# Optimization experiments

Measured on AMD Instinct MI355X. Metric: run time of the kernel, lower is better.

The kernel has to match this reference:

```python
import jax, jax.numpy as jnp
import numpy as np

N_NODES = 100000
N_EDGES = 1600000
IN_DIM = 128
OUT_DIM = 64


def setup_inputs() -> dict:
    key = jax.random.key(0)
    k1, k2, k3, k4 = jax.random.split(key, 4)
    h = jax.random.normal(k1, (N_NODES, IN_DIM), dtype=jnp.float32)
    W = jax.random.normal(k2, (OUT_DIM, IN_DIM), dtype=jnp.float32) * (1.0 / np.sqrt(IN_DIM))
    a_w = jax.random.normal(k3, (1, 2 * OUT_DIM), dtype=jnp.float32) * (1.0 / np.sqrt(2 * OUT_DIM))
    edge_index = jax.random.randint(k4, (2, N_EDGES), 0, N_NODES, dtype=jnp.int64 if jax.config.jax_enable_x64 else jnp.int32)
    return {"h": h, "W": W, "a_w": a_w, "edge_index": edge_index}


def reference(h, W, a_w, edge_index):
    # Wh: [N, out_dim]  (Linear without bias: x @ W.T)
    Wh = h @ W.T
    src, dst = edge_index[0], edge_index[1]
    # per-edge concat [Wh[src], Wh[dst]] -> [E, 2*out_dim]
    e = jnp.concatenate([Wh[src], Wh[dst]], axis=-1)
    # attention logits: [E]
    alpha = jax.nn.leaky_relu(e @ a_w.T, negative_slope=0.2)[:, 0]
    # global-max-stabilized exp (matches the torch code exactly)
    alpha_exp = jnp.exp(alpha - jnp.max(alpha))
    # segment softmax denominator over destination nodes: [N]
    alpha_sum = jax.ops.segment_sum(alpha_exp, dst, num_segments=N_NODES)
    alpha_norm = alpha_exp / (alpha_sum[dst] + 1e-9)
    # weighted scatter-add aggregation: [N, out_dim]
    out = jax.ops.segment_sum(alpha_norm[:, None] * Wh[src], dst, num_segments=N_NODES)
    return (jax.nn.elu(out), alpha_norm)
```

## Files before the change

kernel.cpp:

```cpp
#include <hip/hip_runtime.h>
#include <math.h>

#define N_NODES 100000
#define N_EDGES 1600000
#define IN_DIM 128
#define OUT_DIM 64

#define BSHIFT 9
#define BSIZE  (1 << BSHIFT)
#define NB     ((N_NODES + BSIZE - 1) >> BSHIFT)
#define EDGES_PER_BLK 2048
#define NBLK   ((N_EDGES + EDGES_PER_BLK - 1) / EDGES_PER_BLK)
#define SCANA_LEN (NB * NBLK)
#define SCANA_ITEMS 1024
#define SCANA_NB ((SCANA_LEN + SCANA_ITEMS - 1) / SCANA_ITEMS)

typedef short short8 __attribute__((ext_vector_type(8)));
typedef float f32x4 __attribute__((ext_vector_type(4)));

__device__ __forceinline__ unsigned short f2bf(float x) {
    unsigned int u = __float_as_uint(x);
    return (unsigned short)((u + 0x7FFFu + ((u >> 16) & 1u)) >> 16);
}
__device__ __forceinline__ short8 pack_bf16x8(float4 p, float4 q) {
    short8 r;
    r[0] = (short)f2bf(p.x); r[1] = (short)f2bf(p.y);
    r[2] = (short)f2bf(p.z); r[3] = (short)f2bf(p.w);
    r[4] = (short)f2bf(q.x); r[5] = (short)f2bf(q.y);
    r[6] = (short)f2bf(q.z); r[7] = (short)f2bf(q.w);
    return r;
}

__global__ __launch_bounds__(256) void k_histA(const int* __restrict__ dst,
                                               int* __restrict__ hist_t,
                                               const float* __restrict__ W,
                                               const float* __restrict__ a_w,
                                               float* __restrict__ w1,
                                               float* __restrict__ w2) {
    __shared__ int lhist[NB];
    const int tid = threadIdx.x;
    const int blk = blockIdx.x;
    if (blk == 0 && tid < IN_DIM) {
        float r1 = 0.f, r2 = 0.f;
        #pragma unroll 8
        for (int dd = 0; dd < OUT_DIM; ++dd) {
            float wv = W[dd * IN_DIM + tid];
            r1 = fmaf(a_w[dd], wv, r1);
            r2 = fmaf(a_w[OUT_DIM + dd], wv, r2);
        }
        w1[tid] = r1; w2[tid] = r2;
    }
    if (tid < NB) lhist[tid] = 0;
    __syncthreads();
    const int e0 = blk * EDGES_PER_BLK;
    #pragma unroll
    for (int j = 0; j < 8; ++j) {
        int e = e0 + j * 256 + tid;
        if (e < N_EDGES) atomicAdd(&lhist[dst[e] >> BSHIFT], 1);
    }
    __syncthreads();
    if (tid < NB) hist_t[tid * NBLK + blk] = lhist[tid];
}

__global__ __launch_bounds__(256) void k_wh(const float* __restrict__ h,
                                            const float* __restrict__ W,
                                            const float* __restrict__ w1,
                                            const float* __restrict__ w2,
                                            unsigned short* __restrict__ Wh16,
                                            float* __restrict__ s1,
                                            float* __restrict__ s2) {
    const int tid = threadIdx.x;
    const int wv = tid >> 6;
    const int l  = tid & 63;
    const int g  = l >> 4;
    const int lm = l & 15;
    const int node0 = blockIdx.x * 64 + wv * 16;
    const int row = node0 + lm;
    const int rowc = (row < N_NODES) ? row : (N_NODES - 1);
    const float* hrow = h + (size_t)rowc * IN_DIM;

    short8 afrag[4];
    float sp1 = 0.f, sp2 = 0.f;
    #pragma unroll
    for (int kt = 0; kt < 4; ++kt) {
        const int k0 = kt * 32 + g * 8;
        float4 p = *(const float4*)(hrow + k0);
        float4 q = *(const float4*)(hrow + k0 + 4);
        float4 u1 = *(const float4*)(w1 + k0);
        float4 v1 = *(const float4*)(w1 + k0 + 4);
        float4 u2 = *(const float4*)(w2 + k0);
        float4 v2 = *(const float4*)(w2 + k0 + 4);
        sp1 += p.x*u1.x + p.y*u1.y + p.z*u1.z + p.w*u1.w
             + q.x*v1.x + q.y*v1.y + q.z*v1.z + q.w*v1.w;
        sp2 += p.x*u2.x + p.y*u2.y + p.z*u2.z + p.w*u2.w
             + q.x*v2.x + q.y*v2.y + q.z*v2.z + q.w*v2.w;
        afrag[kt] = pack_bf16x8(p, q);
    }
    sp1 += __shfl_xor(sp1, 16, 64); sp1 += __shfl_xor(sp1, 32, 64);
    sp2 += __shfl_xor(sp2, 16, 64); sp2 += __shfl_xor(sp2, 32, 64);
    if (l < 16 && row < N_NODES) { s1[row] = sp1; s2[row] = sp2; }

    f32x4 acc[4] = {f32x4{0,0,0,0}, f32x4{0,0,0,0}, f32x4{0,0,0,0}, f32x4{0,0,0,0}};
    #pragma unroll
    for (int nt = 0; nt < 4; ++nt) {
        #pragma unroll
        for (int kt = 0; kt < 4; ++kt) {
            const float* wr = W + (size_t)(nt * 16 + lm) * IN_DIM + kt * 32 + g * 8;
            float4 p = *(const float4*)wr;
            float4 q = *(const float4*)(wr + 4);
            short8 bfrag = pack_bf16x8(p, q);
            acc[nt] = __builtin_amdgcn_mfma_f32_16x16x32_bf16(afrag[kt], bfrag, acc[nt], 0, 0, 0);
        }
    }
    #pragma unroll
    for (int nt = 0; nt < 4; ++nt) {
        #pragma unroll
        for (int r = 0; r < 4; ++r) {
            int nodo = node0 + g * 4 + r;
            if (nodo < N_NODES)
                Wh16[(size_t)nodo * OUT_DIM + nt * 16 + lm] = f2bf(acc[nt][r]);
        }
    }
}

__global__ __launch_bounds__(256) void k_scanA_part(const int* __restrict__ in,
                                                    int* __restrict__ bsum) {
    __shared__ int wsum[4];
    const int tid = threadIdx.x;
    const int base = blockIdx.x * SCANA_ITEMS + tid * 4;
    int s = 0;
    #pragma unroll
    for (int j = 0; j < 4; ++j) {
        int i = base + j;
        if (i < SCANA_LEN) s += in[i];
    }
    #pragma unroll
    for (int off = 32; off > 0; off >>= 1) s += __shfl_xor(s, off, 64);
    if ((tid & 63) == 0) wsum[tid >> 6] = s;
    __syncthreads();
    if (tid == 0) bsum[blockIdx.x] = wsum[0] + wsum[1] + wsum[2] + wsum[3];
}

__global__ __launch_bounds__(256) void k_scanA_mid(int* __restrict__ bsum) {
    __shared__ int s[256];
    const int tid = threadIdx.x;
    s[tid] = (tid < SCANA_NB) ? bsum[tid] : 0;
    __syncthreads();
    #pragma unroll
    for (int off = 1; off < 256; off <<= 1) {
        int u = (tid >= off) ? s[tid - off] : 0;
        __syncthreads();
        s[tid] += u;
        __syncthreads();
    }
    if (tid < SCANA_NB) bsum[tid] = (tid > 0) ? s[tid - 1] : 0;
}

__global__ __launch_bounds__(256) void k_scanA_final(const int* __restrict__ in,
                                                     const int* __restrict__ bsum,
                                                     int* __restrict__ outscan) {
    __shared__ int wtot[4];
    const int tid = threadIdx.x;
    const int lane = tid & 63;
    const int wid = tid >> 6;
    const int base = blockIdx.x * SCANA_ITEMS + tid * 4;
    int c[4];
    #pragma unroll
    for (int j = 0; j < 4; ++j)
        c[j] = (base + j < SCANA_LEN) ? in[base + j] : 0;
    int tot = c[0] + c[1] + c[2] + c[3];
    int inc = tot;
    #pragma unroll
    for (int off = 1; off < 64; off <<= 1) {
        int u = __shfl_up(inc, off, 64);
        if (lane >= off) inc += u;
    }
    if (lane == 63) wtot[wid] = inc;
    __syncthreads();
    int wbase = 0;
    #pragma unroll
    for (int w = 0; w < 4; ++w) wbase += (w < wid) ? wtot[w] : 0;
    int run = bsum[blockIdx.x] + wbase + (inc - tot);
    #pragma unroll
    for (int j = 0; j < 4; ++j) {
        int i = base + j;
        if (i < SCANA_LEN) { outscan[i] = run; run += c[j]; }
    }
}

__global__ __launch_bounds__(256) void k_binA(const int* __restrict__ ei,
                                              const float* __restrict__ s1,
                                              const float* __restrict__ s2,
                                              const int* __restrict__ flat_scan,
                                              int2* __restrict__ brec,
                                              float* __restrict__ ae_orig) {
    __shared__ int lbase[NB];
    __shared__ int lcur[NB];
    const int tid = threadIdx.x;
    const int blk = blockIdx.x;
    if (tid < NB) { lbase[tid] = flat_scan[tid * NBLK + blk]; lcur[tid] = 0; }
    __syncthreads();
    const int e0 = blk * EDGES_PER_BLK;
    #pragma unroll
    for (int j = 0; j < 8; ++j) {
        int e = e0 + j * 256 + tid;
        if (e >= N_EDGES) continue;
        int src = ei[e];
        int dst = ei[N_EDGES + e];
        float a = s1[src] + s2[dst];
        a = (a > 0.f) ? a : 0.2f * a;
        float ae = expf(a);
        ae_orig[e] = ae;
        int b = dst >> BSHIFT;
        int r = atomicAdd(&lcur[b], 1);
        brec[lbase[b] + r] = make_int2(src | ((dst & (BSIZE - 1)) << 17),
                                       __float_as_int(ae));
    }
}

__global__ __launch_bounds__(256) void k_fine(const int2* __restrict__ brec,
                                              const int* __restrict__ flat_scan,
                                              int* __restrict__ offsets,
                                              int2* __restrict__ sa_sorted) {
    __shared__ int lhist[BSIZE];
    __shared__ int lofs[BSIZE];
    __shared__ int lcur[BSIZE];
    __shared__ int wsum[4];
    const int tid = threadIdx.x;
    const int lane = tid & 63;
    const int wid = tid >> 6;
    const int b = blockIdx.x;
    const int base = flat_scan[b * NBLK];
    const int endp = (b + 1 < NB) ? flat_scan[(b + 1) * NBLK] : N_EDGES;
    const int cnt = endp - base;
    lhist[tid] = 0; lhist[tid + 256] = 0;
    __syncthreads();
    for (int i = tid; i < cnt; i += 256)
        atomicAdd(&lhist[(unsigned)brec[base + i].x >> 17], 1);
    __syncthreads();
    int c0 = lhist[2 * tid], c1 = lhist[2 * tid + 1];
    int s = c0 + c1;
    int inc = s;
    #pragma unroll
    for (int off = 1; off < 64; off <<= 1) {
        int u = __shfl_up(inc, off, 64);
        if (lane >= off) inc += u;
    }
    if (lane == 63) wsum[wid] = inc;
    __syncthreads();
    int wb = 0;
    #pragma unroll
    for (int w = 0; w < 4; ++w) wb += (w < wid) ? wsum[w] : 0;
    int ex = wb + inc - s;
    lofs[2 * tid] = ex; lofs[2 * tid + 1] = ex + c0;
    lcur[2 * tid] = ex; lcur[2 * tid + 1] = ex + c0;
    __syncthreads();
    const int dst0 = b << BSHIFT;
    #pragma unroll
    for (int j = 0; j < 2; ++j) {
        int jj = tid + j * 256;
        int node = dst0 + jj;
        if (node < N_NODES) offsets[node] = base + lofs[jj];
    }
    if (b == NB - 1 && tid == 0) offsets[N_NODES] = N_EDGES;
    for (int i = tid; i < cnt; i += 256) {
        int2 rec = brec[base + i];
        int dstl = (unsigned)rec.x >> 17;
        int pos = base + atomicAdd(&lcur[dstl], 1);
        sa_sorted[pos] = make_int2(rec.x & 0x1FFFF, rec.y);
    }
}

__global__ __launch_bounds__(256) void k_agg(const int2* __restrict__ sa_sorted,
                                             const int* __restrict__ offsets,
                                             const unsigned short* __restrict__ Wh16,
                                             float* __restrict__ out,
                                             float* __restrict__ inv_tab) {
    const int gid = blockIdx.x * 256 + threadIdx.x;
    const int node = gid >> 6;
    const int l = gid & 63;
    if (node >= N_NODES) return;
    const int g = l >> 3;
    const int o = l & 7;
    const int beg = offsets[node];
    const int end = offsets[node + 1];
    float acc[8] = {0.f, 0.f, 0.f, 0.f, 0.f, 0.f, 0.f, 0.f};
    float S = 0.f;
    int i = beg;
    for (; i + 16 <= end; i += 16) {
        int2 pA = sa_sorted[i + g];
        int2 pB = sa_sorted[i + 8 + g];
        const int4 rA = *(const int4*)(Wh16 + ((size_t)pA.x << 6) + (o << 3));
        const int4 rB = *(const int4*)(Wh16 + ((size_t)pB.x << 6) + (o << 3));
        float aeA = __int_as_float(pA.y);
        float aeB = __int_as_float(pB.y);
        S += aeA + aeB;
        #pragma unroll
        for (int j = 0; j < 4; ++j) {
            int vA = ((const int*)&rA)[j];
            acc[2*j]   = fmaf(aeA, __uint_as_float((unsigned)vA << 16), acc[2*j]);
            acc[2*j+1] = fmaf(aeA, __uint_as_float((unsigned)vA & 0xFFFF0000u), acc[2*j+1]);
        }
        #pragma unroll
        for (int j = 0; j < 4; ++j) {
            int vB = ((const int*)&rB)[j];
            acc[2*j]   = fmaf(aeB, __uint_as_float((unsigned)vB << 16), acc[2*j]);
            acc[2*j+1] = fmaf(aeB, __uint_as_float((unsigned)vB & 0xFFFF0000u), acc[2*j+1]);
        }
    }
    for (; i < end; i += 8) {
        int idx = i + g;
        int2 p = (idx < end) ? sa_sorted[idx] : make_int2(0, 0);
        const int4 r = *(const int4*)(Wh16 + ((size_t)p.x << 6) + (o << 3));
        float ae = __int_as_float(p.y);
        S += ae;
        #pragma unroll
        for (int j = 0; j < 4; ++j) {
            int v = ((const int*)&r)[j];
            acc[2*j]   = fmaf(ae, __uint_as_float((unsigned)v << 16), acc[2*j]);
            acc[2*j+1] = fmaf(ae, __uint_as_float((unsigned)v & 0xFFFF0000u), acc[2*j+1]);
        }
    }
    #pragma unroll
    for (int m = 8; m <= 32; m <<= 1) {
        S += __shfl_xor(S, m, 64);
        #pragma unroll
        for (int j = 0; j < 8; ++j) acc[j] += __shfl_xor(acc[j], m, 64);
    }
    const float inv = 1.f / (S + 1e-9f);
    if (l == 0) inv_tab[node] = inv;
    if (g == 0) {
        float e[8];
        #pragma unroll
        for (int j = 0; j < 8; ++j) {
            float x = acc[j] * inv;
            e[j] = (x > 0.f) ? x : expf(x) - 1.f;
        }
        float* orow = out + (size_t)node * OUT_DIM + o * 8;
        *(float4*)orow = make_float4(e[0], e[1], e[2], e[3]);
        *(float4*)(orow + 4) = make_float4(e[4], e[5], e[6], e[7]);
    }
}

__global__ __launch_bounds__(256) void k_norm(const int* __restrict__ dst_arr,
                                              const float* __restrict__ ae_orig,
                                              const float* __restrict__ inv_tab,
                                              float* __restrict__ alpha_norm) {
    int t = blockIdx.x * 256 + threadIdx.x;
    if (t >= N_EDGES / 4) return;
    int4 d4 = ((const int4*)dst_arr)[t];
    float4 a4 = ((const float4*)ae_orig)[t];
    float4 r;
    r.x = a4.x * inv_tab[d4.x];
    r.y = a4.y * inv_tab[d4.y];
    r.z = a4.z * inv_tab[d4.z];
    r.w = a4.w * inv_tab[d4.w];
    ((float4*)alpha_norm)[t] = r;
}

extern "C" void kernel_launch(void* const* d_in, const int* in_sizes, int n_in,
                              void* d_out, int out_size, void* d_ws, size_t ws_size,
                              hipStream_t stream) {
    const float* h   = (const float*)d_in[0];
    const float* W   = (const float*)d_in[1];
    const float* a_w = (const float*)d_in[2];
    const int*   ei  = (const int*)d_in[3];

    float* out        = (float*)d_out;
    float* alpha_norm = out + (size_t)N_NODES * OUT_DIM;

    char* ws = (char*)d_ws;
    int2* brec      = (int2*)ws;            ws += (size_t)N_EDGES * 8;
    int2* sa_sorted = (int2*)ws;            ws += (size_t)N_EDGES * 8;
    unsigned short* Wh16 = (unsigned short*)ws;  ws += (size_t)N_NODES * OUT_DIM * 2;
    float* ae_orig  = (float*)ws;           ws += (size_t)N_EDGES * 4;
    float* s1       = (float*)ws;           ws += (size_t)N_NODES * 4;
    float* s2       = (float*)ws;           ws += (size_t)N_NODES * 4;
    int*   hist_t   = (int*)ws;             ws += (size_t)SCANA_LEN * 4;
    int*   flat_scan= (int*)ws;             ws += (size_t)SCANA_LEN * 4;
    int*   bsum     = (int*)ws;             ws += (size_t)SCANA_NB * 4;
    int*   offsets  = (int*)ws;             ws += (size_t)(N_NODES + 1) * 4;
    float* inv_tab  = (float*)ws;           ws += (size_t)N_NODES * 4;
    float* w1       = (float*)ws;           ws += (size_t)IN_DIM * 4;
    float* w2       = (float*)ws;           ws += (size_t)IN_DIM * 4;

    k_histA<<<NBLK, 256, 0, stream>>>(ei + N_EDGES, hist_t, W, a_w, w1, w2);
    k_wh<<<(N_NODES + 63) / 64, 256, 0, stream>>>(h, W, w1, w2, Wh16, s1, s2);
    k_scanA_part<<<SCANA_NB, 256, 0, stream>>>(hist_t, bsum);
    k_scanA_mid<<<1, 256, 0, stream>>>(bsum);
    k_scanA_final<<<SCANA_NB, 256, 0, stream>>>(hist_t, bsum, flat_scan);
    k_binA<<<NBLK, 256, 0, stream>>>(ei, s1, s2, flat_scan, brec, ae_orig);
    k_fine<<<NB, 256, 0, stream>>>(brec, flat_scan, offsets, sa_sorted);
    k_agg<<<(N_NODES * 64 + 255) / 256, 256, 0, stream>>>(sa_sorted, offsets, Wh16,
                                                          out, inv_tab);
    k_norm<<<(N_EDGES / 4 + 255) / 256, 256, 0, stream>>>(ei + N_EDGES, ae_orig,
                                                          inv_tab, alpha_norm);
}
```

Before: 164.6 us.

## Fuse fine bucket sort with aggregation using LDS-resident sorted records

New measurement: 170.7 us. 1.04x slower.

```diff
diff --git a/kernel.cpp b/kernel.cpp
--- a/kernel.cpp
+++ b/kernel.cpp
@@ -6,17 +6,19 @@
 #define IN_DIM 128
 #define OUT_DIM 64
 
-#define BSHIFT 9
+#define BSHIFT 7
 #define BSIZE  (1 << BSHIFT)
 #define NB     ((N_NODES + BSIZE - 1) >> BSHIFT)
-#define EDGES_PER_BLK 2048
+#define EDGES_PER_BLK 4096
 #define NBLK   ((N_EDGES + EDGES_PER_BLK - 1) / EDGES_PER_BLK)
 #define SCANA_LEN (NB * NBLK)
 #define SCANA_ITEMS 1024
 #define SCANA_NB ((SCANA_LEN + SCANA_ITEMS - 1) / SCANA_ITEMS)
+#define REC_CAP 3072
 
 typedef short short8 __attribute__((ext_vector_type(8)));
 typedef float f32x4 __attribute__((ext_vector_type(4)));
+typedef float f32x2 __attribute__((ext_vector_type(2)));
 
 __device__ __forceinline__ unsigned short f2bf(float x) {
     unsigned int u = __float_as_uint(x);
@@ -29,6 +31,9 @@
     r[4] = (short)f2bf(q.x); r[5] = (short)f2bf(q.y);
     r[6] = (short)f2bf(q.z); r[7] = (short)f2bf(q.w);
     return r;
+}
+__device__ __forceinline__ void pk_fma(f32x2& d, f32x2 a, f32x2 b) {
+    asm("v_pk_fma_f32 %0, %1, %2, %0" : "+v"(d) : "v"(a), "v"(b));
 }
 
 __global__ __launch_bounds__(256) void k_histA(const int* __restrict__ dst,
@@ -50,16 +55,21 @@
         }
         w1[tid] = r1; w2[tid] = r2;
     }
-    if (tid < NB) lhist[tid] = 0;
+    for (int i = tid; i < NB; i += 256) lhist[i] = 0;
     __syncthreads();
     const int e0 = blk * EDGES_PER_BLK;
     #pragma unroll
-    for (int j = 0; j < 8; ++j) {
-        int e = e0 + j * 256 + tid;
-        if (e < N_EDGES) atomicAdd(&lhist[dst[e] >> BSHIFT], 1);
-    }
-    __syncthreads();
-    if (tid < NB) hist_t[tid * NBLK + blk] = lhist[tid];
+    for (int j = 0; j < 4; ++j) {
+        int e = e0 + (j * 256 + tid) * 4;
+        if (e >= N_EDGES) continue;
+        int4 d4 = *(const int4*)(dst + e);
+        atomicAdd(&lhist[d4.x >> BSHIFT], 1);
+        atomicAdd(&lhist[d4.y >> BSHIFT], 1);
+        atomicAdd(&lhist[d4.z >> BSHIFT], 1);
+        atomicAdd(&lhist[d4.w >> BSHIFT], 1);
+    }
+    __syncthreads();
+    for (int i = tid; i < NB; i += 256) hist_t[i * NBLK + blk] = lhist[i];
 }
 
 __global__ __launch_bounds__(256) void k_wh(const float* __restrict__ h,
@@ -141,13 +151,13 @@
     if (tid == 0) bsum[blockIdx.x] = wsum[0] + wsum[1] + wsum[2] + wsum[3];
 }
 
-__global__ __launch_bounds__(256) void k_scanA_mid(int* __restrict__ bsum) {
-    __shared__ int s[256];
+__global__ __launch_bounds__(512) void k_scanA_mid(int* __restrict__ bsum) {
+    __shared__ int s[512];
     const int tid = threadIdx.x;
     s[tid] = (tid < SCANA_NB) ? bsum[tid] : 0;
     __syncthreads();
     #pragma unroll
-    for (int off = 1; off < 256; off <<= 1) {
+    for (int off = 1; off < 512; off <<= 1) {
         int u = (tid >= off) ? s[tid - off] : 0;
         __syncthreads();
         s[tid] += u;
@@ -198,34 +208,43 @@
     __shared__ int lcur[NB];
     const int tid = threadIdx.x;
     const int blk = blockIdx.x;
-    if (tid < NB) { lbase[tid] = flat_scan[tid * NBLK + blk]; lcur[tid] = 0; }
+    for (int i = tid; i < NB; i += 256) { lbase[i] = flat_scan[i * NBLK + blk]; lcur[i] = 0; }
     __syncthreads();
     const int e0 = blk * EDGES_PER_BLK;
     #pragma unroll
-    for (int j = 0; j < 8; ++j) {
-        int e = e0 + j * 256 + tid;
+    for (int j = 0; j < 4; ++j) {
+        int e = e0 + (j * 256 + tid) * 4;
         if (e >= N_EDGES) continue;
-        int src = ei[e];
-        int dst = ei[N_EDGES + e];
-        float a = s1[src] + s2[dst];
-        a = (a > 0.f) ? a : 0.2f * a;
-        float ae = expf(a);
-        ae_orig[e] = ae;
-        int b = dst >> BSHIFT;
-        int r = atomicAdd(&lcur[b], 1);
-        brec[lbase[b] + r] = make_int2(src | ((dst & (BSIZE - 1)) << 17),
-                                       __float_as_int(ae));
-    }
-}
-
-__global__ __launch_bounds__(256) void k_fine(const int2* __restrict__ brec,
-                                              const int* __restrict__ flat_scan,
-                                              int* __restrict__ offsets,
-                                              int2* __restrict__ sa_sorted) {
+        int4 s4 = *(const int4*)(ei + e);
+        int4 d4 = *(const int4*)(ei + N_EDGES + e);
+        float4 aev;
+        #pragma unroll
+        for (int q = 0; q < 4; ++q) {
+            int src = ((const int*)&s4)[q];
+            int dst = ((const int*)&d4)[q];
+            float a = s1[src] + s2[dst];
+            a = (a > 0.f) ? a : 0.2f * a;
+            float ae = expf(a);
+            ((float*)&aev)[q] = ae;
+            int b = dst >> BSHIFT;
+            int r = atomicAdd(&lcur[b], 1);
+            brec[lbase[b] + r] = make_int2(src | ((dst & (BSIZE - 1)) << 17),
+                                           __float_as_int(ae));
+        }
+        *(float4*)(ae_orig + e) = aev;
+    }
+}
+
+__global__ __launch_bounds__(256) void k_fineagg(const int2* __restrict__ brec,
+                                                 const int* __restrict__ flat_scan,
+                                                 const unsigned short* __restrict__ Wh16,
+                                                 float* __restrict__ out,
+                                                 float* __restrict__ inv_tab) {
+    __shared__ int2 lsorted[REC_CAP];
     __shared__ int lhist[BSIZE];
-    __shared__ int lofs[BSIZE];
+    __shared__ int lofs[BSIZE + 1];
     __shared__ int lcur[BSIZE];
-    __shared__ int wsum[4];
+    __shared__ float linv[BSIZE];
     const int tid = threadIdx.x;
     const int lane = tid & 63;
     const int wid = tid >> 6;
@@ -233,112 +252,113 @@
     const int base = flat_scan[b * NBLK];
     const int endp = (b + 1 < NB) ? flat_scan[(b + 1) * NBLK] : N_EDGES;
     const int cnt = endp - base;
-    lhist[tid] = 0; lhist[tid + 256] = 0;
+    if (tid < BSIZE) lhist[tid] = 0;
     __syncthreads();
     for (int i = tid; i < cnt; i += 256)
         atomicAdd(&lhist[(unsigned)brec[base + i].x >> 17], 1);
     __syncthreads();
-    int c0 = lhist[2 * tid], c1 = lhist[2 * tid + 1];
-    int s = c0 + c1;
-    int inc = s;
-    #pragma unroll
-    for (int off = 1; off < 64; off <<= 1) {
-        int u = __shfl_up(inc, off, 64);
-        if (lane >= off) inc += u;
-    }
-    if (lane == 63) wsum[wid] = inc;
-    __syncthreads();
-    int wb = 0;
-    #pragma unroll
-    for (int w = 0; w < 4; ++w) wb += (w < wid) ? wsum[w] : 0;
-    int ex = wb + inc - s;
-    lofs[2 * tid] = ex; lofs[2 * tid + 1] = ex + c0;
-    lcur[2 * tid] = ex; lcur[2 * tid + 1] = ex + c0;
-    __syncthreads();
-    const int dst0 = b << BSHIFT;
-    #pragma unroll
-    for (int j = 0; j < 2; ++j) {
-        int jj = tid + j * 256;
-        int node = dst0 + jj;
-        if (node < N_NODES) offsets[node] = base + lofs[jj];
-    }
-    if (b == NB - 1 && tid == 0) offsets[N_NODES] = N_EDGES;
+    if (wid == 0) {
+        int c0 = lhist[2 * lane], c1 = lhist[2 * lane + 1];
+        int s = c0 + c1;
+        int inc = s;
+        #pragma unroll
+        for (int off = 1; off < 64; off <<= 1) {
+            int u = __shfl_up(inc, off, 64);
+            if (lane >= off) inc += u;
+        }
+        int ex = inc - s;
+        lofs[2 * lane] = ex; lofs[2 * lane + 1] = ex + c0;
+        lcur[2 * lane] = ex; lcur[2 * lane + 1] = ex + c0;
+        if (lane == 63) lofs[BSIZE] = inc;
+    }
+    __syncthreads();
     for (int i = tid; i < cnt; i += 256) {
         int2 rec = brec[base + i];
         int dstl = (unsigned)rec.x >> 17;
-        int pos = base + atomicAdd(&lcur[dstl], 1);
-        sa_sorted[pos] = make_int2(rec.x & 0x1FFFF, rec.y);
-    }
-}
-
-__global__ __launch_bounds__(256) void k_agg(const int2* __restrict__ sa_sorted,
-                                             const int* __restrict__ offsets,
-                                             const unsigned short* __restrict__ Wh16,
-                                             float* __restrict__ out,
-                                             float* __restrict__ inv_tab) {
-    const int gid = blockIdx.x * 256 + threadIdx.x;
-    const int node = gid >> 6;
-    const int l = gid & 63;
-    if (node >= N_NODES) return;
-    const int g = l >> 3;
-    const int o = l & 7;
-    const int beg = offsets[node];
-    const int end = offsets[node + 1];
-    float acc[8] = {0.f, 0.f, 0.f, 0.f, 0.f, 0.f, 0.f, 0.f};
-    float S = 0.f;
-    int i = beg;
-    for (; i + 16 <= end; i += 16) {
-        int2 pA = sa_sorted[i + g];
-        int2 pB = sa_sorted[i + 8 + g];
-        const int4 rA = *(const int4*)(Wh16 + ((size_t)pA.x << 6) + (o << 3));
-        const int4 rB = *(const int4*)(Wh16 + ((size_t)pB.x << 6) + (o << 3));
-        float aeA = __int_as_float(pA.y);
-        float aeB = __int_as_float(pB.y);
-        S += aeA + aeB;
+        int pos = atomicAdd(&lcur[dstl], 1);
+        lsorted[pos] = make_int2(rec.x & 0x1FFFF, rec.y);
+    }
+    __syncthreads();
+    const int g = lane >> 3;
+    const int o = lane & 7;
+    const int dst0 = b << BSHIFT;
+    for (int j = 0; j < 32; ++j) {
+        const int bin = wid * 32 + j;
+        const int node = dst0 + bin;
+        if (node >= N_NODES) break;
+        const int beg = lofs[bin];
+        const int end2 = lofs[bin + 1];
+        f32x2 acc2[4] = {f32x2{0,0}, f32x2{0,0}, f32x2{0,0}, f32x2{0,0}};
+        float S = 0.f;
+        int i = beg;
+        for (; i + 16 <= end2; i += 16) {
+            int2 pA = lsorted[i + g];
+            int2 pB = lsorted[i + 8 + g];
+            const int4 rA = *(const int4*)(Wh16 + ((size_t)pA.x << 6) + (o << 3));
+            const int4 rB = *(const int4*)(Wh16 + ((size_t)pB.x << 6) + (o << 3));
+            float aeA = __int_as_float(pA.y);
+            float aeB = __int_as_float(pB.y);
+            S += aeA + aeB;
+            f32x2 a2A = {aeA, aeA}, a2B = {aeB, aeB};
+            #pragma unroll
+            for (int q = 0; q < 4; ++q) {
+                int v = ((const int*)&rA)[q];
+                f32x2 f = { __uint_as_float((unsigned)v << 16),
+                            __uint_as_float((unsigned)v & 0xFFFF0000u) };
+                pk_fma(acc2[q], f, a2A);
+            }
+            #pragma unroll
+            for (int q = 0; q < 4; ++q) {
+                int v = ((const int*)&rB)[q];
+                f32x2 f = { __uint_as_float((unsigned)v << 16),
+                            __uint_as_float((unsigned)v & 0xFFFF0000u) };
+                pk_fma(acc2[q], f, a2B);
+            }
+        }
+        for (; i < end2; i += 8) {
+            int idx = i + g;
+            int2 p = (idx < end2) ? lsorted[idx] : make_int2(0, 0);
+            const int4 r = *(const int4*)(Wh16 + ((size_t)p.x << 6) + (o << 3));
+            float ae = __int_as_float(p.y);
+            S += ae;
+            f32x2 a2 = {ae, ae};
+            #pragma unroll
+            for (int q = 0; q < 4; ++q) {
+                int v = ((const int*)&r)[q];
+                f32x2 f = { __uint_as_float((unsigned)v << 16),
+                            __uint_as_float((unsigned)v & 0xFFFF0000u) };
+                pk_fma(acc2[q], f, a2);
+            }
+        }
         #pragma unroll
-        for (int j = 0; j < 4; ++j) {
-            int vA = ((const int*)&rA)[j];
-            acc[2*j]   = fmaf(aeA, __uint_as_float((unsigned)vA << 16), acc[2*j]);
-            acc[2*j+1] = fmaf(aeA, __uint_as_float((unsigned)vA & 0xFFFF0000u), acc[2*j+1]);
-        }
-        #pragma unroll
-        for (int j = 0; j < 4; ++j) {
-            int vB = ((const int*)&rB)[j];
-            acc[2*j]   = fmaf(aeB, __uint_as_float((unsigned)vB << 16), acc[2*j]);
-            acc[2*j+1] = fmaf(aeB, __uint_as_float((unsigned)vB & 0xFFFF0000u), acc[2*j+1]);
-        }
-    }
-    for (; i < end; i += 8) {
-        int idx = i + g;
-        int2 p = (idx < end) ? sa_sorted[idx] : make_int2(0, 0);
-        const int4 r = *(const int4*)(Wh16 + ((size_t)p.x << 6) + (o << 3));
-        float ae = __int_as_float(p.y);
-        S += ae;
-        #pragma unroll
-        for (int j = 0; j < 4; ++j) {
-            int v = ((const int*)&r)[j];
-            acc[2*j]   = fmaf(ae, __uint_as_float((unsigned)v << 16), acc[2*j]);
-            acc[2*j+1] = fmaf(ae, __uint_as_float((unsigned)v & 0xFFFF0000u), acc[2*j+1]);
-        }
-    }
-    #pragma unroll
-    for (int m = 8; m <= 32; m <<= 1) {
-        S += __shfl_xor(S, m, 64);
-        #pragma unroll
-        for (int j = 0; j < 8; ++j) acc[j] += __shfl_xor(acc[j], m, 64);
-    }
-    const float inv = 1.f / (S + 1e-9f);
-    if (l == 0) inv_tab[node] = inv;
-    if (g == 0) {
-        float e[8];
-        #pragma unroll
-        for (int j = 0; j < 8; ++j) {
-            float x = acc[j] * inv;
-            e[j] = (x > 0.f) ? x : expf(x) - 1.f;
-        }
-        float* orow = out + (size_t)node * OUT_DIM + o * 8;
-        *(float4*)orow = make_float4(e[0], e[1], e[2], e[3]);
-        *(float4*)(orow + 4) = make_float4(e[4], e[5], e[6], e[7]);
+        for (int m = 8; m <= 32; m <<= 1) {
+            S += __shfl_xor(S, m, 64);
+            #pragma unroll
+            for (int q = 0; q < 4; ++q) {
+                acc2[q].x += __shfl_xor(acc2[q].x, m, 64);
+                acc2[q].y += __shfl_xor(acc2[q].y, m, 64);
+            }
+        }
+        const float inv = 1.f / (S + 1e-9f);
+        if (lane == 0) linv[bin] = inv;
+        if (g == 0) {
+            float e[8];
+            #pragma unroll
+            for (int q = 0; q < 4; ++q) {
+                float x0 = acc2[q].x * inv;
+                float x1 = acc2[q].y * inv;
+                e[2*q]   = (x0 > 0.f) ? x0 : expf(x0) - 1.f;
+                e[2*q+1] = (x1 > 0.f) ? x1 : expf(x1) - 1.f;
+            }
+            float* orow = out + (size_t)node * OUT_DIM + o * 8;
+            *(float4*)orow = make_float4(e[0], e[1], e[2], e[3]);
+            *(float4*)(orow + 4) = make_float4(e[4], e[5], e[6], e[7]);
+        }
+    }
+    __syncthreads();
+    if (tid < BSIZE) {
+        int node = dst0 + tid;
+        if (node < N_NODES) inv_tab[node] = linv[tid];
     }
 }
 
@@ -371,7 +391,6 @@
 
     char* ws = (char*)d_ws;
     int2* brec      = (int2*)ws;            ws += (size_t)N_EDGES * 8;
-    int2* sa_sorted = (int2*)ws;            ws += (size_t)N_EDGES * 8;
     unsigned short* Wh16 = (unsigned short*)ws;  ws += (size_t)N_NODES * OUT_DIM * 2;
     float* ae_orig  = (float*)ws;           ws += (size_t)N_EDGES * 4;
     float* s1       = (float*)ws;           ws += (size_t)N_NODES * 4;
@@ -379,7 +398,6 @@
     int*   hist_t   = (int*)ws;             ws += (size_t)SCANA_LEN * 4;
     int*   flat_scan= (int*)ws;             ws += (size_t)SCANA_LEN * 4;
     int*   bsum     = (int*)ws;             ws += (size_t)SCANA_NB * 4;
-    int*   offsets  = (int*)ws;             ws += (size_t)(N_NODES + 1) * 4;
     float* inv_tab  = (float*)ws;           ws += (size_t)N_NODES * 4;
     float* w1       = (float*)ws;           ws += (size_t)IN_DIM * 4;
     float* w2       = (float*)ws;           ws += (size_t)IN_DIM * 4;
@@ -387,12 +405,10 @@
     k_histA<<<NBLK, 256, 0, stream>>>(ei + N_EDGES, hist_t, W, a_w, w1, w2);
     k_wh<<<(N_NODES + 63) / 64, 256, 0, stream>>>(h, W, w1, w2, Wh16, s1, s2);
     k_scanA_part<<<SCANA_NB, 256, 0, stream>>>(hist_t, bsum);
-    k_scanA_mid<<<1, 256, 0, stream>>>(bsum);
+    k_scanA_mid<<<1, 512, 0, stream>>>(bsum);
     k_scanA_final<<<SCANA_NB, 256, 0, stream>>>(hist_t, bsum, flat_scan);
     k_binA<<<NBLK, 256, 0, stream>>>(ei, s1, s2, flat_scan, brec, ae_orig);
-    k_fine<<<NB, 256, 0, stream>>>(brec, flat_scan, offsets, sa_sorted);
-    k_agg<<<(N_NODES * 64 + 255) / 256, 256, 0, stream>>>(sa_sorted, offsets, Wh16,
-                                                          out, inv_tab);
+    k_fineagg<<<NB, 256, 0, stream>>>(brec, flat_scan, Wh16, out, inv_tab);
     k_norm<<<(N_EDGES / 4 + 255) / 256, 256, 0, stream>>>(ei + N_EDGES, ae_orig,
                                                           inv_tab, alpha_norm);
 }
```
